# Kernel optimization log

Hardware: AMD Instinct MI355X
Metric: run time of the kernel (lower is better)

Reference implementation:

```python
import jax, jax.numpy as jnp
import numpy as np

NUM_HEADS = 16


def setup_inputs() -> dict:
    key = jax.random.key(0)
    ks = jax.random.split(key, 5)
    B, S, D = 2, 2048, 1024
    scale = 1.0 / np.sqrt(D)
    return {
        "hidden_states": jax.random.normal(ks[0], (B, S, D), dtype=jnp.float32),
        "Wq": jax.random.normal(ks[1], (D, D), dtype=jnp.float32) * scale,
        "bq": jnp.zeros((D,), jnp.float32),
        "Wk": jax.random.normal(ks[2], (D, D), dtype=jnp.float32) * scale,
        "bk": jnp.zeros((D,), jnp.float32),
        "Wv": jax.random.normal(ks[3], (D, D), dtype=jnp.float32) * scale,
        "bv": jnp.zeros((D,), jnp.float32),
        "Wo": jax.random.normal(ks[4], (D, D), dtype=jnp.float32) * scale,
        "bo": jnp.zeros((D,), jnp.float32),
    }


def reference(hidden_states, Wq, bq, Wk, bk, Wv, bv, Wo, bo):
    B, S, D = hidden_states.shape
    H = NUM_HEADS
    Dh = D // H

    def split_heads(x):  # [B,S,D] -> [B,H,S,Dh]
        return x.reshape(B, S, H, Dh).transpose(0, 2, 1, 3)

    q = split_heads(hidden_states @ Wq + bq)
    k = split_heads(hidden_states @ Wk + bk)
    v = split_heads(hidden_states @ Wv + bv)

    # causal additive mask: -inf strictly above the diagonal (triu, diagonal=1)
    i = jnp.arange(S)
    causal = jnp.where(i[None, :] > i[:, None], -jnp.inf, 0.0).astype(hidden_states.dtype)  # [S,S]

    scores = jnp.einsum("bhsd,bhtd->bhst", q, k) / jnp.sqrt(jnp.asarray(Dh, hidden_states.dtype))
    scores = scores + causal[None, None, :, :]
    weights = jax.nn.softmax(scores, axis=-1)  # [B,H,S,S]
    ctx = jnp.einsum("bhst,bhtd->bhsd", weights, v)
    ctx = ctx.transpose(0, 2, 1, 3).reshape(B, S, D)
    return ctx @ Wo + bo
```

## Files before the change

### kernel.cpp

```cpp
#include <hip/hip_runtime.h>
#include <math.h>

#define SEQ    2048
#define DMODEL 1024
#define NHEADS 16
#define DHEAD  64
#define NBATCH 2

typedef __attribute__((ext_vector_type(8)))  short bf16x8;
typedef __attribute__((ext_vector_type(4)))  float f32x4;
typedef __attribute__((ext_vector_type(16))) float f32x16;

__device__ __forceinline__ unsigned short f2bf(float f) {
    union { float f; unsigned u; } v; v.f = f;
    unsigned r = (v.u + 0x7FFF + ((v.u >> 16) & 1)) >> 16;
    return (unsigned short)r;
}

__device__ __forceinline__ unsigned cvt_pk_bf16(float lo, float hi) {
    unsigned r;
    asm("v_cvt_pk_bf16_f32 %0, %1, %2" : "=v"(r) : "v"(lo), "v"(hi));
    return r;
}

__global__ __launch_bounds__(256)
void cast_bf16_kernel(const float* __restrict__ in, unsigned short* __restrict__ out) {
    const size_t g8 = ((size_t)blockIdx.x * 256 + threadIdx.x) * 8;
    float4 a = *reinterpret_cast<const float4*>(in + g8);
    float4 b = *reinterpret_cast<const float4*>(in + g8 + 4);
    bf16x8 o;
    o[0] = (short)f2bf(a.x); o[1] = (short)f2bf(a.y);
    o[2] = (short)f2bf(a.z); o[3] = (short)f2bf(a.w);
    o[4] = (short)f2bf(b.x); o[5] = (short)f2bf(b.y);
    o[6] = (short)f2bf(b.z); o[7] = (short)f2bf(b.w);
    *reinterpret_cast<bf16x8*>(out + g8) = o;
}

__global__ __launch_bounds__(256)
void wt_cast_kernel(const float* __restrict__ W, unsigned short* __restrict__ Wt) {
    __shared__ float tile[64][65];
    const int nt  = blockIdx.x & 15;
    const int kt  = blockIdx.x >> 4;
    const int tid = threadIdx.x;

#pragma unroll
    for (int r = 0; r < 4; ++r) {
        int kl = r * 16 + (tid >> 4);
        int nl = (tid & 15) * 4;
        float4 v = *reinterpret_cast<const float4*>(
            &W[(size_t)(kt * 64 + kl) * 1024 + nt * 64 + nl]);
        tile[kl][nl + 0] = v.x; tile[kl][nl + 1] = v.y;
        tile[kl][nl + 2] = v.z; tile[kl][nl + 3] = v.w;
    }
    __syncthreads();

    const int n  = tid >> 2;
    const int kc = (tid & 3) * 16;
    bf16x8 o0, o1;
#pragma unroll
    for (int i = 0; i < 8; ++i) o0[i] = (short)f2bf(tile[kc + i][n]);
#pragma unroll
    for (int i = 0; i < 8; ++i) o1[i] = (short)f2bf(tile[kc + 8 + i][n]);
    unsigned short* op = Wt + (size_t)(nt * 64 + n) * 1024 + kt * 64 + kc;
    *reinterpret_cast<bf16x8*>(op)     = o0;
    *reinterpret_cast<bf16x8*>(op + 8) = o1;
}

template <int MODE>
__global__ __launch_bounds__(256)
void gemm_bf16(const unsigned short* __restrict__ A,
               const unsigned short* __restrict__ Bt,
               const float* __restrict__ bias0, const float* __restrict__ bias1,
               const float* __restrict__ bias2,
               float* __restrict__ Cf,
               unsigned short* __restrict__ Qo, unsigned short* __restrict__ Ko,
               unsigned short* __restrict__ Vo,
               int M, int N, int K) {
    __shared__ unsigned short As[128 * 40];
    __shared__ unsigned short Bs[128 * 40];

    const int tid  = threadIdx.x;
    const int bm   = blockIdx.y * 128;
    const int bn   = blockIdx.x * 128;
    const int w    = tid >> 6;
    const int lane = tid & 63;
    const int lrow = lane & 15;
    const int lk   = lane >> 4;
    const int wm0  = (w >> 1) * 64;
    const int wn0  = (w & 1) * 64;

    const int sr = tid >> 2;
    const int sc = tid & 3;

    const unsigned short* Ag = A  + (size_t)bm * K;
    const unsigned short* Bg = Bt + (size_t)bn * K;

    f32x4 acc[4][4];
#pragma unroll
    for (int i = 0; i < 4; ++i)
#pragma unroll
        for (int j = 0; j < 4; ++j) acc[i][j] = (f32x4){0.f, 0.f, 0.f, 0.f};

    bf16x8 ra0, ra1, rb0, rb1;
    {
        const int k = sc * 8;
        ra0 = *reinterpret_cast<const bf16x8*>(Ag + (size_t)sr * K + k);
        ra1 = *reinterpret_cast<const bf16x8*>(Ag + (size_t)(64 + sr) * K + k);
        rb0 = *reinterpret_cast<const bf16x8*>(Bg + (size_t)sr * K + k);
        rb1 = *reinterpret_cast<const bf16x8*>(Bg + (size_t)(64 + sr) * K + k);
    }
    *reinterpret_cast<bf16x8*>(&As[sr * 40 + sc * 8])        = ra0;
    *reinterpret_cast<bf16x8*>(&As[(64 + sr) * 40 + sc * 8]) = ra1;
    *reinterpret_cast<bf16x8*>(&Bs[sr * 40 + sc * 8])        = rb0;
    *reinterpret_cast<bf16x8*>(&Bs[(64 + sr) * 40 + sc * 8]) = rb1;
    __syncthreads();

    const int NT = K / 32;
    for (int kt = 0; kt < NT; ++kt) {
        if (kt + 1 < NT) {
            const int k = (kt + 1) * 32 + sc * 8;
            ra0 = *reinterpret_cast<const bf16x8*>(Ag + (size_t)sr * K + k);
            ra1 = *reinterpret_cast<const bf16x8*>(Ag + (size_t)(64 + sr) * K + k);
            rb0 = *reinterpret_cast<const bf16x8*>(Bg + (size_t)sr * K + k);
            rb1 = *reinterpret_cast<const bf16x8*>(Bg + (size_t)(64 + sr) * K + k);
        }
        bf16x8 af[4], bf[4];
#pragma unroll
        for (int mg = 0; mg < 4; ++mg)
            af[mg] = *reinterpret_cast<const bf16x8*>(
                &As[(wm0 + mg * 16 + lrow) * 40 + lk * 8]);
#pragma unroll
        for (int ng = 0; ng < 4; ++ng)
            bf[ng] = *reinterpret_cast<const bf16x8*>(
                &Bs[(wn0 + ng * 16 + lrow) * 40 + lk * 8]);
#pragma unroll
        for (int mg = 0; mg < 4; ++mg)
#pragma unroll
            for (int ng = 0; ng < 4; ++ng)
                acc[mg][ng] = __builtin_amdgcn_mfma_f32_16x16x32_bf16(
                    af[mg], bf[ng], acc[mg][ng], 0, 0, 0);
        __syncthreads();
        if (kt + 1 < NT) {
            *reinterpret_cast<bf16x8*>(&As[sr * 40 + sc * 8])        = ra0;
            *reinterpret_cast<bf16x8*>(&As[(64 + sr) * 40 + sc * 8]) = ra1;
            *reinterpret_cast<bf16x8*>(&Bs[sr * 40 + sc * 8])        = rb0;
            *reinterpret_cast<bf16x8*>(&Bs[(64 + sr) * 40 + sc * 8]) = rb1;
            __syncthreads();
        }
    }

    if (MODE == 0) {
        const int type = bn >> 10;
        const int nloc = bn & 1023;
        const float* bias = (type == 0) ? bias0 : (type == 1) ? bias1 : bias2;
        const float QSCALE = 0.125f * 1.44269504088896f;
#pragma unroll
        for (int ng = 0; ng < 4; ++ng) {
            const int col = nloc + wn0 + ng * 16 + lrow;
            const float bv = bias[col];
            const int h = col >> 6, d = col & 63;
#pragma unroll
            for (int mg = 0; mg < 4; ++mg) {
#pragma unroll
                for (int j = 0; j < 4; ++j) {
                    const int row = bm + wm0 + mg * 16 + lk * 4 + j;
                    const int b = row >> 11, s = row & 2047;
                    const float val = acc[mg][ng][j] + bv;
                    if (type == 0)
                        Qo[((size_t)(b * 16 + h) * SEQ + s) * 64 + d] = f2bf(val * QSCALE);
                    else if (type == 1)
                        Ko[((size_t)(b * 16 + h) * SEQ + s) * 64 + d] = f2bf(val);
                    else
                        Vo[((size_t)(b * 16 + h) * 64 + d) * SEQ + s] = f2bf(val);
                }
            }
        }
    } else {
#pragma unroll
        for (int ng = 0; ng < 4; ++ng) {
            const int col = bn + wn0 + ng * 16 + lrow;
            const float bv = bias0[col];
#pragma unroll
            for (int mg = 0; mg < 4; ++mg) {
#pragma unroll
                for (int j = 0; j < 4; ++j) {
                    const int row = bm + wm0 + mg * 16 + lk * 4 + j;
                    Cf[(size_t)row * N + col] = acc[mg][ng][j] + bv;
                }
            }
        }
    }
}

__global__ __launch_bounds__(256)
void attn_mfma_kernel(const unsigned short* __restrict__ Qg,
                      const unsigned short* __restrict__ Kg,
                      const unsigned short* __restrict__ Vtg,
                      unsigned short* __restrict__ CTX) {
    __shared__ __align__(16) unsigned short Ks[2][64 * 64];
    __shared__ __align__(16) unsigned short Vt[2][64 * 64];

    const int bid = blockIdx.x;
    const int bh  = bid >> 4;
    const int pos = bid & 15;
    const int dir = ((bid >> 4) ^ (bid >> 8)) & 1;
    const int rb  = dir ? pos : (15 - pos);
    const int b  = bh >> 4;
    const int h  = bh & 15;
    const int r0 = rb * 128;
    const int tid  = threadIdx.x;
    const int w    = tid >> 6;
    const int lane = tid & 63;
    const int qcol = lane & 31;
    const int hlf  = lane >> 5;
    const int wr0  = r0 + w * 32;
    const int qrow = wr0 + qcol;

    const unsigned short* Kb = Kg + ((size_t)bh * SEQ) * DHEAD;
    const unsigned short* Vb = Vtg + ((size_t)bh * DHEAD) * SEQ;

    bf16x8 qf[4];
    {
        const unsigned short* qp = Qg + ((size_t)bh * SEQ + qrow) * DHEAD + hlf * 8;
#pragma unroll
        for (int ksub = 0; ksub < 4; ++ksub)
            qf[ksub] = *reinterpret_cast<const bf16x8*>(qp + ksub * 16);
    }

    f32x16 O0, O1;
#pragma unroll
    for (int r = 0; r < 16; ++r) { O0[r] = 0.f; O1[r] = 0.f; }
    float m = -1e30f, l = 0.f;

    const int srow = tid >> 2;
    const int c0   = (tid & 3) * 16;
    const int sb0  = srow * 128 + ((c0 * 2) ^ ((srow & 7) << 4));
    const int sb1  = srow * 128 + (((c0 + 8) * 2) ^ ((srow & 7) << 4));

    bf16x8 rk0, rk1, rv0, rv1;
    {
        const unsigned short* kp = Kb + (size_t)srow * DHEAD + c0;
        const unsigned short* vp = Vb + (size_t)srow * SEQ + c0;
        rk0 = *reinterpret_cast<const bf16x8*>(kp);
        rk1 = *reinterpret_cast<const bf16x8*>(kp + 8);
        rv0 = *reinterpret_cast<const bf16x8*>(vp);
        rv1 = *reinterpret_cast<const bf16x8*>(vp + 8);
    }

    const int ntile = (r0 + 128) / 64;
    for (int t = 0; t < ntile; ++t) {
        const int j0 = t * 64;
        const int buf = t & 1;
        *reinterpret_cast<bf16x8*>((char*)&Ks[buf][0] + sb0) = rk0;
        *reinterpret_cast<bf16x8*>((char*)&Ks[buf][0] + sb1) = rk1;
        *reinterpret_cast<bf16x8*>((char*)&Vt[buf][0] + sb0) = rv0;
        *reinterpret_cast<bf16x8*>((char*)&Vt[buf][0] + sb1) = rv1;
        __syncthreads();
        if (t + 1 < ntile) {
            const int j1 = j0 + 64;
            const unsigned short* kp = Kb + (size_t)(j1 + srow) * DHEAD + c0;
            const unsigned short* vp = Vb + (size_t)srow * SEQ + j1 + c0;
            rk0 = *reinterpret_cast<const bf16x8*>(kp);
            rk1 = *reinterpret_cast<const bf16x8*>(kp + 8);
            rv0 = *reinterpret_cast<const bf16x8*>(vp);
            rv1 = *reinterpret_cast<const bf16x8*>(vp + 8);
        }

        if (j0 <= wr0 + 31) {
            f32x16 S[2];
#pragma unroll
            for (int r = 0; r < 16; ++r) { S[0][r] = 0.f; S[1][r] = 0.f; }
            __builtin_amdgcn_s_setprio(1);
#pragma unroll
            for (int kb = 0; kb < 2; ++kb) {
                const int key = kb * 32 + qcol;
#pragma unroll
                for (int ksub = 0; ksub < 4; ++ksub) {
                    int boff = key * 128 + ((ksub * 32 + hlf * 16) ^ ((key & 7) << 4));
                    bf16x8 kf = *reinterpret_cast<const bf16x8*>((char*)&Ks[buf][0] + boff);
                    S[kb] = __builtin_amdgcn_mfma_f32_32x32x16_bf16(
                        kf, qf[ksub], S[kb], 0, 0, 0);
                }
            }
            __builtin_amdgcn_s_setprio(0);

            if (j0 + 63 > wr0) {
#pragma unroll
                for (int kb = 0; kb < 2; ++kb)
#pragma unroll
                    for (int r = 0; r < 16; ++r) {
                        int ka = j0 + kb * 32 + (r & 3) + 8 * (r >> 2) + 4 * hlf;
                        if (ka > qrow) S[kb][r] = -1e30f;
                    }
            }

            float pm = S[0][0];
#pragma unroll
            for (int r = 1; r < 16; ++r) pm = fmaxf(pm, S[0][r]);
#pragma unroll
            for (int r = 0; r < 16; ++r) pm = fmaxf(pm, S[1][r]);
            pm = fmaxf(pm, __shfl_xor(pm, 32));

            if (__any(pm > m)) {
                float mnew = fmaxf(m, pm);
                float cor  = __builtin_amdgcn_exp2f(m - mnew);
                m = mnew;
                l *= cor;
#pragma unroll
                for (int r = 0; r < 16; ++r) { O0[r] *= cor; O1[r] *= cor; }
            }

            float ls = 0.f;
#pragma unroll
            for (int kb = 0; kb < 2; ++kb)
#pragma unroll
                for (int r = 0; r < 16; ++r) {
                    float p = __builtin_amdgcn_exp2f(S[kb][r] - m);
                    S[kb][r] = p;
                    ls += p;
                }
            l += ls;

#pragma unroll
            for (int kc = 0; kc < 4; ++kc) {
                const int kb = kc >> 1;
                const int R0 = (kc & 1) * 8;
                unsigned pa = cvt_pk_bf16(S[kb][R0 + 0], S[kb][R0 + 1]);
                unsigned pc = cvt_pk_bf16(S[kb][R0 + 4], S[kb][R0 + 5]);
                asm("v_permlane32_swap_b32 %0, %1" : "+v"(pa), "+v"(pc));
                unsigned pb = cvt_pk_bf16(S[kb][R0 + 2], S[kb][R0 + 3]);
                unsigned pd = cvt_pk_bf16(S[kb][R0 + 6], S[kb][R0 + 7]);
                asm("v_permlane32_swap_b32 %0, %1" : "+v"(pb), "+v"(pd));
                union { unsigned u[4]; bf16x8 v; } pf;
                pf.u[0] = pa; pf.u[1] = pb; pf.u[2] = pc; pf.u[3] = pd;
                __builtin_amdgcn_s_setprio(1);
#pragma unroll
                for (int db = 0; db < 2; ++db) {
                    const int dim = db * 32 + qcol;
                    int boff = dim * 128 + ((kc * 32 + hlf * 16) ^ ((dim & 7) << 4));
                    bf16x8 vf = *reinterpret_cast<const bf16x8*>((char*)&Vt[buf][0] + boff);
                    if (db == 0)
                        O0 = __builtin_amdgcn_mfma_f32_32x32x16_bf16(vf, pf.v, O0, 0, 0, 0);
                    else
                        O1 = __builtin_amdgcn_mfma_f32_32x32x16_bf16(vf, pf.v, O1, 0, 0, 0);
                }
                __builtin_amdgcn_s_setprio(0);
            }
        }
    }

    l += __shfl_xor(l, 32);
    const float inv = 1.f / l;
    unsigned short* crow = CTX + ((size_t)(b * SEQ + qrow)) * DMODEL + h * DHEAD;
#pragma unroll
    for (int pq = 0; pq < 4; ++pq) {
        unsigned w0 = cvt_pk_bf16(O0[pq * 4 + 0] * inv, O0[pq * 4 + 1] * inv);
        unsigned w1 = cvt_pk_bf16(O0[pq * 4 + 2] * inv, O0[pq * 4 + 3] * inv);
        uint2 val; val.x = w0; val.y = w1;
        *reinterpret_cast<uint2*>(crow + 8 * pq + 4 * hlf) = val;
    }
#pragma unroll
    for (int pq = 0; pq < 4; ++pq) {
        unsigned w0 = cvt_pk_bf16(O1[pq * 4 + 0] * inv, O1[pq * 4 + 1] * inv);
        unsigned w1 = cvt_pk_bf16(O1[pq * 4 + 2] * inv, O1[pq * 4 + 3] * inv);
        uint2 val; val.x = w0; val.y = w1;
        *reinterpret_cast<uint2*>(crow + 32 + 8 * pq + 4 * hlf) = val;
    }
}

extern "C" void kernel_launch(void* const* d_in, const int* in_sizes, int n_in,
                              void* d_out, int out_size, void* d_ws, size_t ws_size,
                              hipStream_t stream) {
    const float* hs = (const float*)d_in[0];
    const float* Wq = (const float*)d_in[1];
    const float* bq = (const float*)d_in[2];
    const float* Wk = (const float*)d_in[3];
    const float* bk = (const float*)d_in[4];
    const float* Wv = (const float*)d_in[5];
    const float* bv = (const float*)d_in[6];
    const float* Wo = (const float*)d_in[7];
    const float* bo = (const float*)d_in[8];
    float* out = (float*)d_out;

    const size_t NTOK = (size_t)NBATCH * SEQ;
    unsigned short* hs_bf  = (unsigned short*)d_ws;
    unsigned short* Wqkv_t = hs_bf + NTOK * DMODEL;
    unsigned short* Wo_t   = Wqkv_t + 3072 * 1024;
    unsigned short* Qh     = Wo_t + 1024 * 1024;
    unsigned short* Kh     = Qh + NTOK * DMODEL;
    unsigned short* Vt     = Kh + NTOK * DMODEL;
    unsigned short* Cb     = Vt + NTOK * DMODEL;

    cast_bf16_kernel<<<(int)(NTOK * DMODEL / 8 / 256), 256, 0, stream>>>(hs, hs_bf);
    wt_cast_kernel<<<256, 256, 0, stream>>>(Wq, Wqkv_t);
    wt_cast_kernel<<<256, 256, 0, stream>>>(Wk, Wqkv_t + 1024 * 1024);
    wt_cast_kernel<<<256, 256, 0, stream>>>(Wv, Wqkv_t + 2 * 1024 * 1024);
    wt_cast_kernel<<<256, 256, 0, stream>>>(Wo, Wo_t);

    dim3 gqkv(3072 / 128, NTOK / 128);
    gemm_bf16<0><<<gqkv, 256, 0, stream>>>(hs_bf, Wqkv_t, bq, bk, bv,
                                           nullptr, Qh, Kh, Vt,
                                           (int)NTOK, 3072, DMODEL);

    attn_mfma_kernel<<<NBATCH * NHEADS * (SEQ / 128), 256, 0, stream>>>(Qh, Kh, Vt, Cb);

    dim3 go(DMODEL / 128, NTOK / 128);
    gemm_bf16<1><<<go, 256, 0, stream>>>(Cb, Wo_t, bo, nullptr, nullptr,
                                         out, nullptr, nullptr, nullptr,
                                         (int)NTOK, DMODEL, DMODEL);
}
```

Measured before the change: 135.9 us.

## Use direct global-to-LDS loads in GEMM, remap attention blocks, tree-reduce softmax

The GEMM now loads tiles straight into LDS with global_load_lds and an XOR-swizzled layout in place of the register-staged double-buffer and padded rows. This removes the VGPR round trip and the padding, but it also drops the overlap between global prefetch and MFMA, since loads are now issued and awaited in the same iteration. The attention kernel remaps block IDs so the same head sits on one XCD and interleaves causal row-block order. The softmax max and sum reductions are split into independent chains to shorten dependency latency.

```diff
diff --git a/kernel.cpp b/kernel.cpp
--- a/kernel.cpp
+++ b/kernel.cpp
@@ -21,6 +21,12 @@
     unsigned r;
     asm("v_cvt_pk_bf16_f32 %0, %1, %2" : "=v"(r) : "v"(lo), "v"(hi));
     return r;
+}
+
+__device__ __forceinline__ void gload16(const void* g, void* l) {
+    __builtin_amdgcn_global_load_lds(
+        (const __attribute__((address_space(1))) unsigned*)g,
+        (__attribute__((address_space(3))) unsigned*)l, 16, 0, 0);
 }
 
 __global__ __launch_bounds__(256)
@@ -76,8 +82,8 @@
                unsigned short* __restrict__ Qo, unsigned short* __restrict__ Ko,
                unsigned short* __restrict__ Vo,
                int M, int N, int K) {
-    __shared__ unsigned short As[128 * 40];
-    __shared__ unsigned short Bs[128 * 40];
+    __shared__ unsigned short As[128 * 32];
+    __shared__ unsigned short Bs[128 * 32];
 
     const int tid  = threadIdx.x;
     const int bm   = blockIdx.y * 128;
@@ -89,8 +95,13 @@
     const int wm0  = (w >> 1) * 64;
     const int wn0  = (w & 1) * 64;
 
-    const int sr = tid >> 2;
-    const int sc = tid & 3;
+    const int boff0 = tid * 16;
+    const int boff1 = 4096 + tid * 16;
+    const int row0  = tid >> 2;
+    const int row1  = 64 + row0;
+    const int c     = tid & 3;
+    const int sw0   = (c ^ ((row0 >> 1) & 3)) * 8;
+    const int sw1   = (c ^ ((row1 >> 1) & 3)) * 8;
 
     const unsigned short* Ag = A  + (size_t)bm * K;
     const unsigned short* Bg = Bt + (size_t)bn * K;
@@ -101,38 +112,28 @@
 #pragma unroll
         for (int j = 0; j < 4; ++j) acc[i][j] = (f32x4){0.f, 0.f, 0.f, 0.f};
 
-    bf16x8 ra0, ra1, rb0, rb1;
-    {
-        const int k = sc * 8;
-        ra0 = *reinterpret_cast<const bf16x8*>(Ag + (size_t)sr * K + k);
-        ra1 = *reinterpret_cast<const bf16x8*>(Ag + (size_t)(64 + sr) * K + k);
-        rb0 = *reinterpret_cast<const bf16x8*>(Bg + (size_t)sr * K + k);
-        rb1 = *reinterpret_cast<const bf16x8*>(Bg + (size_t)(64 + sr) * K + k);
-    }
-    *reinterpret_cast<bf16x8*>(&As[sr * 40 + sc * 8])        = ra0;
-    *reinterpret_cast<bf16x8*>(&As[(64 + sr) * 40 + sc * 8]) = ra1;
-    *reinterpret_cast<bf16x8*>(&Bs[sr * 40 + sc * 8])        = rb0;
-    *reinterpret_cast<bf16x8*>(&Bs[(64 + sr) * 40 + sc * 8]) = rb1;
-    __syncthreads();
-
     const int NT = K / 32;
     for (int kt = 0; kt < NT; ++kt) {
-        if (kt + 1 < NT) {
-            const int k = (kt + 1) * 32 + sc * 8;
-            ra0 = *reinterpret_cast<const bf16x8*>(Ag + (size_t)sr * K + k);
-            ra1 = *reinterpret_cast<const bf16x8*>(Ag + (size_t)(64 + sr) * K + k);
-            rb0 = *reinterpret_cast<const bf16x8*>(Bg + (size_t)sr * K + k);
-            rb1 = *reinterpret_cast<const bf16x8*>(Bg + (size_t)(64 + sr) * K + k);
-        }
+        const int k0 = kt * 32;
+        gload16(Ag + (size_t)row0 * K + k0 + sw0, (char*)As + boff0);
+        gload16(Ag + (size_t)row1 * K + k0 + sw1, (char*)As + boff1);
+        gload16(Bg + (size_t)row0 * K + k0 + sw0, (char*)Bs + boff0);
+        gload16(Bg + (size_t)row1 * K + k0 + sw1, (char*)Bs + boff1);
+        __syncthreads();
+
         bf16x8 af[4], bf[4];
 #pragma unroll
-        for (int mg = 0; mg < 4; ++mg)
+        for (int mg = 0; mg < 4; ++mg) {
+            const int r = wm0 + mg * 16 + lrow;
             af[mg] = *reinterpret_cast<const bf16x8*>(
-                &As[(wm0 + mg * 16 + lrow) * 40 + lk * 8]);
-#pragma unroll
-        for (int ng = 0; ng < 4; ++ng)
+                (char*)As + r * 64 + ((lk ^ ((r >> 1) & 3)) * 16));
+        }
+#pragma unroll
+        for (int ng = 0; ng < 4; ++ng) {
+            const int r = wn0 + ng * 16 + lrow;
             bf[ng] = *reinterpret_cast<const bf16x8*>(
-                &Bs[(wn0 + ng * 16 + lrow) * 40 + lk * 8]);
+                (char*)Bs + r * 64 + ((lk ^ ((r >> 1) & 3)) * 16));
+        }
 #pragma unroll
         for (int mg = 0; mg < 4; ++mg)
 #pragma unroll
@@ -140,13 +141,6 @@
                 acc[mg][ng] = __builtin_amdgcn_mfma_f32_16x16x32_bf16(
                     af[mg], bf[ng], acc[mg][ng], 0, 0, 0);
         __syncthreads();
-        if (kt + 1 < NT) {
-            *reinterpret_cast<bf16x8*>(&As[sr * 40 + sc * 8])        = ra0;
-            *reinterpret_cast<bf16x8*>(&As[(64 + sr) * 40 + sc * 8]) = ra1;
-            *reinterpret_cast<bf16x8*>(&Bs[sr * 40 + sc * 8])        = rb0;
-            *reinterpret_cast<bf16x8*>(&Bs[(64 + sr) * 40 + sc * 8]) = rb1;
-            __syncthreads();
-        }
     }
 
     if (MODE == 0) {
@@ -163,7 +157,7 @@
             for (int mg = 0; mg < 4; ++mg) {
 #pragma unroll
                 for (int j = 0; j < 4; ++j) {
-                    const int row = bm + wm0 + mg * 16 + lk * 4 + j;
+                    const int row = bm + wm0 + mg * 16 + (lane >> 4) * 4 + j;
                     const int b = row >> 11, s = row & 2047;
                     const float val = acc[mg][ng][j] + bv;
                     if (type == 0)
@@ -184,7 +178,7 @@
             for (int mg = 0; mg < 4; ++mg) {
 #pragma unroll
                 for (int j = 0; j < 4; ++j) {
-                    const int row = bm + wm0 + mg * 16 + lk * 4 + j;
+                    const int row = bm + wm0 + mg * 16 + (lane >> 4) * 4 + j;
                     Cf[(size_t)row * N + col] = acc[mg][ng][j] + bv;
                 }
             }
@@ -200,11 +194,12 @@
     __shared__ __align__(16) unsigned short Ks[2][64 * 64];
     __shared__ __align__(16) unsigned short Vt[2][64 * 64];
 
-    const int bid = blockIdx.x;
-    const int bh  = bid >> 4;
-    const int pos = bid & 15;
-    const int dir = ((bid >> 4) ^ (bid >> 8)) & 1;
-    const int rb  = dir ? pos : (15 - pos);
+    const int bid  = blockIdx.x;
+    const int xcd  = bid & 7;
+    const int slot = bid >> 3;
+    const int bh   = (slot >> 4) * 8 + xcd;
+    const int rb_i = slot & 15;
+    const int rb   = (rb_i & 1) ? (15 - (rb_i >> 1)) : (rb_i >> 1);
     const int b  = bh >> 4;
     const int h  = bh & 15;
     const int r0 = rb * 128;
@@ -294,11 +289,14 @@
                     }
             }
 
-            float pm = S[0][0];
-#pragma unroll
-            for (int r = 1; r < 16; ++r) pm = fmaxf(pm, S[0][r]);
-#pragma unroll
-            for (int r = 0; r < 16; ++r) pm = fmaxf(pm, S[1][r]);
+            float mx[8];
+#pragma unroll
+            for (int r = 0; r < 8; ++r)
+                mx[r] = fmaxf(fmaxf(S[0][r], S[0][r + 8]),
+                              fmaxf(S[1][r], S[1][r + 8]));
+            float m01 = fmaxf(mx[0], mx[1]), m23 = fmaxf(mx[2], mx[3]);
+            float m45 = fmaxf(mx[4], mx[5]), m67 = fmaxf(mx[6], mx[7]);
+            float pm = fmaxf(fmaxf(m01, m23), fmaxf(m45, m67));
             pm = fmaxf(pm, __shfl_xor(pm, 32));
 
             if (__any(pm > m)) {
@@ -310,16 +308,20 @@
                 for (int r = 0; r < 16; ++r) { O0[r] *= cor; O1[r] *= cor; }
             }
 
-            float ls = 0.f;
+            float l0 = 0.f, l1 = 0.f, l2 = 0.f, l3 = 0.f;
 #pragma unroll
             for (int kb = 0; kb < 2; ++kb)
 #pragma unroll
-                for (int r = 0; r < 16; ++r) {
-                    float p = __builtin_amdgcn_exp2f(S[kb][r] - m);
-                    S[kb][r] = p;
-                    ls += p;
+                for (int r = 0; r < 16; r += 4) {
+                    float p0 = __builtin_amdgcn_exp2f(S[kb][r + 0] - m);
+                    float p1 = __builtin_amdgcn_exp2f(S[kb][r + 1] - m);
+                    float p2 = __builtin_amdgcn_exp2f(S[kb][r + 2] - m);
+                    float p3 = __builtin_amdgcn_exp2f(S[kb][r + 3] - m);
+                    S[kb][r + 0] = p0; S[kb][r + 1] = p1;
+                    S[kb][r + 2] = p2; S[kb][r + 3] = p3;
+                    l0 += p0; l1 += p1; l2 += p2; l3 += p3;
                 }
-            l += ls;
+            l += (l0 + l1) + (l2 + l3);
 
 #pragma unroll
             for (int kc = 0; kc < 4; ++kc) {
```

After: 153.8 us. 1.13x slower.
